# Kernel optimization log

Measured on AMD Instinct MI355X. Metric: run time of the kernel, lower is better.

Reference implementation:

```python
import jax, jax.numpy as jnp
import numpy as np


def setup_inputs() -> dict:
    key = jax.random.key(0)
    k1, k2 = jax.random.split(key)
    B, C, H, W = 4, 64, 256, 512
    right_input = jax.random.normal(k1, (B, C, H, W), dtype=jnp.float32)
    disparity_samples = jax.random.uniform(k2, (B, 1, H, W), dtype=jnp.float32)
    return {"right_input": right_input, "disparity_samples": disparity_samples}


def reference(right_input, disparity_samples):
    B, C, H, W = right_input.shape
    dt = right_input.dtype
    # left pixel x-coordinates along width, broadcast over B,1,H
    left_y = jnp.arange(W, dtype=dt).reshape(1, 1, 1, W)
    right_y = left_y + disparity_samples                      # [B,1,H,W]
    ry_a = jnp.floor(right_y)
    ry_b = ry_a + 1.0
    wa = ry_b - right_y                                       # [B,1,H,W]
    wb = right_y - ry_a
    idx_a = jnp.clip(ry_a, 0, W - 1).astype(jnp.int32)
    idx_b = jnp.clip(ry_b, 0, W - 1).astype(jnp.int32)
    # broadcast indices across channels and gather along width (dim=3)
    idx_a = jnp.broadcast_to(idx_a, (B, C, H, W))
    idx_b = jnp.broadcast_to(idx_b, (B, C, H, W))
    feat_a = jnp.take_along_axis(right_input, idx_a, axis=3)
    feat_b = jnp.take_along_axis(right_input, idx_b, axis=3)
    warped = wa * feat_a + wb * feat_b                        # weights broadcast over C
    # zero out samples whose (unclamped) coordinate fell outside [0, W-1]
    oob = (right_y < 0).astype(dt) + (right_y > (W - 1)).astype(dt)
    return (1.0 - oob) * warped
```

## Files before the change

kernel.cpp:

```cpp
#include <hip/hip_runtime.h>

constexpr int B = 4;
constexpr int C = 64;
constexpr int H = 256;
constexpr int W = 512;
constexpr int CH_PER_BLOCK = 16;
constexpr int WAVES = 4;
constexpr int CH_PER_WAVE = CH_PER_BLOCK / WAVES;

__global__ __launch_bounds__(256) void spatial_warp_kernel(
    const float* __restrict__ input,
    const float* __restrict__ disp,
    float* __restrict__ out)
{
    __shared__ float s_rows[WAVES][2][W];

    const int t    = threadIdx.x;
    const int lane = t & 63;
    const int wid  = t >> 6;

    const int cg = blockIdx.x % (C / CH_PER_BLOCK);
    int rest     = blockIdx.x / (C / CH_PER_BLOCK);
    const int h  = rest % H;
    const int b  = rest / H;
    const int c0 = cg * CH_PER_BLOCK + wid * CH_PER_WAVE;

    const long long pix = ((long long)b * H + h) * (long long)W;

    float waf[8], wbf[8];
    int   addr0[8];
    const float* drow = disp + pix;
#pragma unroll
    for (int j = 0; j < 8; ++j) {
        const int w   = lane + 64 * j;
        const float d  = drow[w];
        const float ry = (float)w + d;
        const float ra = floorf(ry);
        const float wa = ra + 1.0f - ry;
        const float wb = ry - ra;
        const float msk = (ry >= 0.0f && ry <= (float)(W - 1)) ? 1.0f : 0.0f;
        const float iaf = fminf(fmaxf(ra, 0.0f), (float)(W - 1));
        const int   ia  = (int)iaf;
        const bool  hi  = (ia >= W - 1);
        const int   i0  = hi ? (W - 2) : ia;
        waf[j]   = hi ? 0.0f : msk * wa;
        wbf[j]   = hi ? msk  : msk * wb;
        addr0[j] = i0 * 4;
    }

    const long long chStride = (long long)H * W;
    const float* grow = input + ((long long)(b * C + c0)) * chStride + pix % ((long long)H * W)
                        ;
    grow = input + (((long long)b * C + c0) * H + h) * (long long)W;
    float* orow = out + (((long long)b * C + c0) * H + h) * (long long)W;

    float4 v0 = reinterpret_cast<const float4*>(grow)[lane];
    float4 v1 = reinterpret_cast<const float4*>(grow)[64 + lane];

#pragma unroll
    for (int cc = 0; cc < CH_PER_WAVE; ++cc) {
        float* buf = &s_rows[wid][cc & 1][0];
        reinterpret_cast<float4*>(buf)[lane]      = v0;
        reinterpret_cast<float4*>(buf)[64 + lane] = v1;

        if (cc + 1 < CH_PER_WAVE) {
            const float* gnext = grow + (long long)(cc + 1) * chStride;
            v0 = reinterpret_cast<const float4*>(gnext)[lane];
            v1 = reinterpret_cast<const float4*>(gnext)[64 + lane];
        }

        asm volatile("s_waitcnt lgkmcnt(0)" ::: "memory");

        float* op = orow + (long long)cc * chStride;
#pragma unroll
        for (int j = 0; j < 8; ++j) {
            const float fa = *reinterpret_cast<const float*>(
                reinterpret_cast<const char*>(buf) + addr0[j]);
            const float fb = *reinterpret_cast<const float*>(
                reinterpret_cast<const char*>(buf) + addr0[j] + 4);
            op[lane + 64 * j] = waf[j] * fa + wbf[j] * fb;
        }
    }
}

extern "C" void kernel_launch(void* const* d_in, const int* in_sizes, int n_in,
                              void* d_out, int out_size, void* d_ws, size_t ws_size,
                              hipStream_t stream) {
    const float* input = (const float*)d_in[0];
    const float* disp  = (const float*)d_in[1];
    float* outp = (float*)d_out;

    const int grid = B * H * (C / CH_PER_BLOCK);
    spatial_warp_kernel<<<grid, 256, 0, stream>>>(input, disp, outp);
}
```

Baseline: 240.4 us.

## Replace LDS row staging with direct global gathers and nontemporal stores

Drops the shared-memory staging of each input row. Each thread now handles one pixel column and gathers its two neighbours directly from global memory for 16 channels, relying on L1/L2 locality because the disparity is small. Blocks grow to 512 threads, the disparity math is done once per thread, and outputs are written with nontemporal stores. The risk is that scattered gathers are less efficient than coalesced float4 loads plus LDS reads.

```diff
diff --git a/kernel.cpp b/kernel.cpp
--- a/kernel.cpp
+++ b/kernel.cpp
@@ -4,82 +4,50 @@
 constexpr int C = 64;
 constexpr int H = 256;
 constexpr int W = 512;
-constexpr int CH_PER_BLOCK = 16;
-constexpr int WAVES = 4;
-constexpr int CH_PER_WAVE = CH_PER_BLOCK / WAVES;
+constexpr int CPB = 16;
+constexpr long long HW = (long long)H * W;
 
-__global__ __launch_bounds__(256) void spatial_warp_kernel(
+__global__ __launch_bounds__(512) void spatial_warp_kernel(
     const float* __restrict__ input,
     const float* __restrict__ disp,
     float* __restrict__ out)
 {
-    __shared__ float s_rows[WAVES][2][W];
-
-    const int t    = threadIdx.x;
-    const int lane = t & 63;
-    const int wid  = t >> 6;
-
-    const int cg = blockIdx.x % (C / CH_PER_BLOCK);
-    int rest     = blockIdx.x / (C / CH_PER_BLOCK);
-    const int h  = rest % H;
-    const int b  = rest / H;
-    const int c0 = cg * CH_PER_BLOCK + wid * CH_PER_WAVE;
+    const int w    = threadIdx.x;
+    const int cg   = blockIdx.x & (C / CPB - 1);
+    const int rest = blockIdx.x >> 2;
+    const int h    = rest & (H - 1);
+    const int b    = rest >> 8;
 
     const long long pix = ((long long)b * H + h) * (long long)W;
 
-    float waf[8], wbf[8];
-    int   addr0[8];
-    const float* drow = disp + pix;
+    const float d   = disp[pix + w];
+    const float ry  = (float)w + d;
+    const float ra  = floorf(ry);
+    const float wa  = ra + 1.0f - ry;
+    const float wb  = ry - ra;
+    const float msk = (ry >= 0.0f && ry <= (float)(W - 1)) ? 1.0f : 0.0f;
+    const float iaf = fminf(fmaxf(ra, 0.0f), (float)(W - 1));
+    const int   ia  = (int)iaf;
+    const bool  hi  = (ia >= W - 1);
+    const int   i0  = hi ? (W - 2) : ia;
+    const float waf = hi ? 0.0f : msk * wa;
+    const float wbf = hi ? msk  : msk * wb;
+
+    const int c0 = cg * CPB;
+    const float* p = input + (((long long)b * C + c0) * H + h) * (long long)W;
+    float*       q = out   + (((long long)b * C + c0) * H + h) * (long long)W + w;
+
+    float va[CPB], vb[CPB];
 #pragma unroll
-    for (int j = 0; j < 8; ++j) {
-        const int w   = lane + 64 * j;
-        const float d  = drow[w];
-        const float ry = (float)w + d;
-        const float ra = floorf(ry);
-        const float wa = ra + 1.0f - ry;
-        const float wb = ry - ra;
-        const float msk = (ry >= 0.0f && ry <= (float)(W - 1)) ? 1.0f : 0.0f;
-        const float iaf = fminf(fmaxf(ra, 0.0f), (float)(W - 1));
-        const int   ia  = (int)iaf;
-        const bool  hi  = (ia >= W - 1);
-        const int   i0  = hi ? (W - 2) : ia;
-        waf[j]   = hi ? 0.0f : msk * wa;
-        wbf[j]   = hi ? msk  : msk * wb;
-        addr0[j] = i0 * 4;
+    for (int cc = 0; cc < CPB; ++cc) {
+        const float* row = p + (long long)cc * HW;
+        va[cc] = row[i0];
+        vb[cc] = row[i0 + 1];
     }
-
-    const long long chStride = (long long)H * W;
-    const float* grow = input + ((long long)(b * C + c0)) * chStride + pix % ((long long)H * W)
-                        ;
-    grow = input + (((long long)b * C + c0) * H + h) * (long long)W;
-    float* orow = out + (((long long)b * C + c0) * H + h) * (long long)W;
-
-    float4 v0 = reinterpret_cast<const float4*>(grow)[lane];
-    float4 v1 = reinterpret_cast<const float4*>(grow)[64 + lane];
-
 #pragma unroll
-    for (int cc = 0; cc < CH_PER_WAVE; ++cc) {
-        float* buf = &s_rows[wid][cc & 1][0];
-        reinterpret_cast<float4*>(buf)[lane]      = v0;
-        reinterpret_cast<float4*>(buf)[64 + lane] = v1;
-
-        if (cc + 1 < CH_PER_WAVE) {
-            const float* gnext = grow + (long long)(cc + 1) * chStride;
-            v0 = reinterpret_cast<const float4*>(gnext)[lane];
-            v1 = reinterpret_cast<const float4*>(gnext)[64 + lane];
-        }
-
-        asm volatile("s_waitcnt lgkmcnt(0)" ::: "memory");
-
-        float* op = orow + (long long)cc * chStride;
-#pragma unroll
-        for (int j = 0; j < 8; ++j) {
-            const float fa = *reinterpret_cast<const float*>(
-                reinterpret_cast<const char*>(buf) + addr0[j]);
-            const float fb = *reinterpret_cast<const float*>(
-                reinterpret_cast<const char*>(buf) + addr0[j] + 4);
-            op[lane + 64 * j] = waf[j] * fa + wbf[j] * fb;
-        }
+    for (int cc = 0; cc < CPB; ++cc) {
+        __builtin_nontemporal_store(waf * va[cc] + wbf * vb[cc],
+                                    q + (long long)cc * HW);
     }
 }
 
@@ -90,6 +58,6 @@
     const float* disp  = (const float*)d_in[1];
     float* outp = (float*)d_out;
 
-    const int grid = B * H * (C / CH_PER_BLOCK);
-    spatial_warp_kernel<<<grid, 256, 0, stream>>>(input, disp, outp);
+    const int grid = B * H * (C / CPB);
+    spatial_warp_kernel<<<grid, 512, 0, stream>>>(input, disp, outp);
 }
```

Measured after the change: 240.2 us. No clear change (-0.1%).
